# Kernel tuning notes

Measured on AMD Instinct MI355X. Metric: run time of the kernel, lower is better.

The kernel has to match this reference:

```python
import jax, jax.numpy as jnp
import numpy as np

VOCAB = 32000
D = 256        # embedding dim
NB = 256       # n_bubbles
NEQ = 5        # n_equilibrium_steps
THRESH = 1.5   # surprise_threshold
SEQ = 64
DECAYS = np.array([0.3, 0.7, 0.9], dtype=np.float32)  # RunningKnow frame decay rates


def setup_inputs() -> dict:
    key = jax.random.key(0)
    k1, k2, k3 = jax.random.split(key, 3)
    tokens = jax.random.randint(k1, (SEQ,), 0, VOCAB)
    E = jax.random.normal(k2, (VOCAB, D), dtype=jnp.float32)
    # Foam bubble measurement operators (stand-in: per-bubble linear map), scaled for sane stats
    W = jax.random.normal(k3, (NB, D, D), dtype=jnp.float32) / np.float32(np.sqrt(D))
    return {
        "tokens": tokens,
        "E": E,
        "W": W,
        "memory_decay_base": jnp.asarray(0.8, dtype=jnp.float32),
        "novelty_sensitivity": jnp.asarray(1.0, dtype=jnp.float32),
    }


def _equilibrate(m):
    # Stand-in for Foam.equilibrate: NEQ relaxation steps toward the bubble mean.
    for _ in range(NEQ):
        m = m + 0.1 * (m.mean(axis=0, keepdims=True) - m)
    return m


def reference(tokens, E, W, memory_decay_base, novelty_sensitivity):
    dr = jnp.asarray(DECAYS)[:, None, None]          # [F,1,1]
    F = dr.shape[0]
    sens = jnp.abs(novelty_sensitivity)

    def step(carry, tok):
        memory, means, vars_, n_seen = carry
        x = E[tok]                                   # [D]
        mm = memory.mean(axis=0)                     # [D]
        mem_norm = jnp.linalg.norm(mm) + 1e-10
        x_norm = jnp.linalg.norm(x) + 1e-10
        novelty = jnp.where(mem_norm > 1e-8,
                            1.0 - jnp.dot(x, mm) / (x_norm * mem_norm),
                            jnp.float32(1.0))
        decay = jax.nn.sigmoid(memory_decay_base - sens * novelty)
        xm = x + decay * mm                          # [D]

        meas = jnp.einsum('d,nde->ne', xm, W)        # [NB,D] bubble measurements

        # RunningKnow.evaluate (blank model at n_seen==0 -> never knows)
        std = jnp.sqrt(vars_ + 1e-8)                 # [F,NB,D]
        surprise = (jnp.abs(meas[None] - means) / std).mean(axis=(1, 2))  # [F]
        any_knows = jnp.any((surprise < THRESH) & (n_seen > 0))

        eq = _equilibrate(meas)
        eff = jnp.where(any_knows, meas, eq)         # know -> skip equilibration
        eff_d = jax.lax.stop_gradient(eff)           # .detach() in torch

        # RunningKnow.update (EMA mean/var per frame; first call initializes)
        upd_mean = dr * means + (1.0 - dr) * eff_d
        upd_var = jnp.maximum(dr * vars_ + (1.0 - dr) * (eff_d - means) * (eff_d - upd_mean), 1e-8)
        first = (n_seen == 0)
        means = jnp.where(first, jnp.broadcast_to(eff_d, (F, NB, D)), upd_mean)
        vars_ = jnp.where(first, jnp.float32(0.1), upd_var)

        # density matrix and spectrum
        mnorm = eff / (jnp.linalg.norm(eff, axis=-1, keepdims=True) + 1e-10)  # [NB,D]
        rho = mnorm.T @ mnorm / NB                   # [D,D]
        eigs = jnp.linalg.eigvalsh(jax.lax.stop_gradient(rho))
        eigs = jnp.maximum(eigs, 1e-12)
        eigs = eigs / eigs.sum()

        memory = decay * memory + (1.0 - decay) * eff_d
        logits = ((E @ rho) * E).sum(axis=-1)        # [VOCAB]
        return (memory, means, vars_, n_seen + 1), (logits, eigs)

    carry0 = (jnp.zeros((NB, D), jnp.float32),
              jnp.zeros((F, NB, D), jnp.float32),
              jnp.ones((F, NB, D), jnp.float32),
              jnp.int32(0))
    _, (logits, eigs) = jax.lax.scan(step, carry0, tokens)
    return logits, eigs  # [SEQ,VOCAB], [SEQ,D]
```

## Files before the change

### kernel.cpp

```cpp
#include <hip/hip_runtime.h>
#include <hip/hip_bf16.h>
#include <cstdint>
#include <cstddef>

constexpr size_t OFF_MEM    = 0;
constexpr size_t OFF_XM     = 65536;
constexpr size_t OFF_MU     = 82176;
constexpr size_t OFF_SABS   = 98560;
constexpr size_t OFF_BAR    = 98816;
constexpr size_t ZERO_END   = 98880;
constexpr size_t OFF_WBAR   = 98880;
constexpr size_t OFF_MEANS  = 164416;
constexpr size_t OFF_VARS   = 361024;
constexpr size_t OFF_DT     = 557632;
constexpr size_t OFF_ET     = 574016;
constexpr size_t OFF_RHO    = 590400;
constexpr size_t OFF_MN16   = 4784704;
constexpr size_t OFF_E16    = 6881856;
constexpr size_t WS_FLOATS  = 10977856;

#define SEQ_ 64
#define VOCAB_ 32000

typedef __attribute__((ext_vector_type(8))) short bf16x8;
typedef __attribute__((ext_vector_type(4))) float f32x4;

__device__ __forceinline__ float wave_sum(float v){
  v += __shfl_xor(v, 32); v += __shfl_xor(v, 16); v += __shfl_xor(v, 8);
  v += __shfl_xor(v, 4);  v += __shfl_xor(v, 2);  v += __shfl_xor(v, 1);
  return v;
}
__device__ __forceinline__ float block_sum(float v, float* red){
  int tid = threadIdx.x;
  v = wave_sum(v);
  if ((tid & 63) == 0) red[tid >> 6] = v;
  __syncthreads();
  float r = red[0] + red[1] + red[2] + red[3];
  __syncthreads();
  return r;
}
__device__ __forceinline__ float block_min(float v, float* red){
  int tid = threadIdx.x;
  v = fminf(v, __shfl_xor(v, 32)); v = fminf(v, __shfl_xor(v, 16));
  v = fminf(v, __shfl_xor(v, 8));  v = fminf(v, __shfl_xor(v, 4));
  v = fminf(v, __shfl_xor(v, 2));  v = fminf(v, __shfl_xor(v, 1));
  if ((tid & 63) == 0) red[tid >> 6] = v;
  __syncthreads();
  float r = fminf(fminf(red[0], red[1]), fminf(red[2], red[3]));
  __syncthreads();
  return r;
}
__device__ __forceinline__ float block_max(float v, float* red){
  int tid = threadIdx.x;
  v = fmaxf(v, __shfl_xor(v, 32)); v = fmaxf(v, __shfl_xor(v, 16));
  v = fmaxf(v, __shfl_xor(v, 8));  v = fmaxf(v, __shfl_xor(v, 4));
  v = fmaxf(v, __shfl_xor(v, 2));  v = fmaxf(v, __shfl_xor(v, 1));
  if ((tid & 63) == 0) red[tid >> 6] = v;
  __syncthreads();
  float r = fmaxf(fmaxf(red[0], red[1]), fmaxf(red[2], red[3]));
  __syncthreads();
  return r;
}

__global__ __launch_bounds__(256) void k0_init(const float* __restrict__ E, float* __restrict__ ws){
  size_t i = (size_t)blockIdx.x * 256 + threadIdx.x;
  if (i < ZERO_END) ws[i] = 0.f;
  __hip_bfloat16* e16 = (__hip_bfloat16*)(ws + OFF_E16);
  e16[i] = __float2bfloat16(E[i]);
}

__global__ __launch_bounds__(256) void k_wbar(const float* __restrict__ W, float* __restrict__ ws){
  size_t i = (size_t)blockIdx.x * 256 + threadIdx.x;
  float s = 0.f;
  #pragma unroll 4
  for (int n = 0; n < 256; ++n)
    s += W[(size_t)n * 65536 + i];
  ws[OFF_WBAR + i] = s * (1.0f / 256.0f);
}

__global__ __launch_bounds__(1024, 1) void k_xm(const int* __restrict__ tokens,
    const float* __restrict__ E, const float* __restrict__ mdbp,
    const float* __restrict__ nsp, float* __restrict__ ws){
  __shared__ float xm_s[256];
  __shared__ __align__(16) float part[4][256];
  __shared__ float redA[16], redB[16], redC[16];
  const int tid = threadIdx.x;
  const int e = tid & 255, q = tid >> 8;
  const int lane = tid & 63, w = tid >> 6;
  const float sens = fabsf(nsp[0]);
  const float mdb  = mdbp[0];
  const float* Wb = ws + OFF_WBAR;
  float mm = 0.f;

  float wreg[64];
  {
    const float* Wq = Wb + (size_t)(q * 64) * 256 + e;
    #pragma unroll
    for (int dd = 0; dd < 64; ++dd)
      wreg[dd] = Wq[(size_t)dd * 256];
  }

  for (int t = 0; t < SEQ_; ++t){
    int tok = tokens[t];
    float xv = (tid < 256) ? E[(size_t)tok * 256 + e] : 0.f;
    float a = wave_sum(xv * mm);
    float b = wave_sum(xv * xv);
    float c = wave_sum(mm * mm);
    if (lane == 0){ redA[w] = a; redB[w] = b; redC[w] = c; }
    __syncthreads();
    float sdot = (redA[0] + redA[1]) + (redA[2] + redA[3]);
    float sx2  = (redB[0] + redB[1]) + (redB[2] + redB[3]);
    float sm2  = (redC[0] + redC[1]) + (redC[2] + redC[3]);
    float mem_norm = sqrtf(sm2) + 1e-10f;
    float x_norm   = sqrtf(sx2) + 1e-10f;
    float novelty = (mem_norm > 1e-8f) ? (1.0f - sdot / (x_norm * mem_norm)) : 1.0f;
    float z = mdb - sens * novelty;
    float decay = 1.0f / (1.0f + expf(-z));
    if (tid < 256){
      float xmv = xv + decay * mm;
      xm_s[e] = xmv;
      ws[OFF_XM + (size_t)e * 64 + t] = xmv;
    }
    __syncthreads();

    float p = 0.f;
    #pragma unroll
    for (int dd = 0; dd < 64; ++dd)
      p = fmaf(xm_s[q * 64 + dd], wreg[dd], p);
    part[q][e] = p;
    __syncthreads();
    if (tid < 256){
      float acc = (part[0][e] + part[1][e]) + (part[2][e] + part[3][e]);
      ws[OFF_MU + (size_t)t * 256 + e] = acc;
      mm = decay * mm + (1.0f - decay) * acc;
    }
    __syncthreads();
  }
}

__global__ __launch_bounds__(256) void k_measall(const float* __restrict__ W, float* __restrict__ ws){
  __shared__ __align__(16) float xm_s[16384];
  const int tid = threadIdx.x, n = blockIdx.x;
  for (int i = tid; i < 16384; i += 256) xm_s[i] = ws[OFF_XM + i];
  __syncthreads();

  float acc[64];
  #pragma unroll
  for (int t = 0; t < 64; ++t) acc[t] = 0.f;

  const float* Wn = W + (size_t)n * 65536 + tid;
  for (int d = 0; d < 256; ++d){
    float wv = Wn[(size_t)d * 256];
    const float* xr = &xm_s[d * 64];
    #pragma unroll
    for (int q = 0; q < 16; ++q){
      float4 x4 = *(const float4*)&xr[q * 4];
      acc[q * 4 + 0] = fmaf(x4.x, wv, acc[q * 4 + 0]);
      acc[q * 4 + 1] = fmaf(x4.y, wv, acc[q * 4 + 1]);
      acc[q * 4 + 2] = fmaf(x4.z, wv, acc[q * 4 + 2]);
      acc[q * 4 + 3] = fmaf(x4.w, wv, acc[q * 4 + 3]);
    }
  }
  #pragma unroll
  for (int t = 0; t < 64; ++t)
    ws[OFF_RHO + (size_t)n * 16384 + (size_t)t * 256 + tid] = acc[t];
}

__global__ __launch_bounds__(1024, 1) void k_stats(float* __restrict__ ws){
  __shared__ float redA[16], redB[16], redC[16];
  const int tid = threadIdx.x;
  const int e = tid & 255, q = tid >> 8;
  const int lane = tid & 63, w = tid >> 6;
  const int n = blockIdx.x * 4 + q;
  unsigned* bar = (unsigned*)(ws + OFF_BAR);
  __hip_bfloat16* mn16 = (__hip_bfloat16*)(ws + OFF_MN16);
  const size_t ne = (size_t)n * 256 + e;
  const float TH = 1.5f * 65536.0f;
  const float c5 = 0.59049f;

  float mean0 = 0.f, mean1 = 0.f, mean2 = 0.f;
  float var0 = 0.f, var1 = 0.f, var2 = 0.f;

  for (int t = 0; t < SEQ_; ++t){
    float me = ws[OFF_RHO + (size_t)n * 16384 + (size_t)t * 256 + e];
    bool know = false;
    if (t > 0){
      float v0 = fabsf(me - mean0) / sqrtf(var0 + 1e-8f);
      float v1 = fabsf(me - mean1) / sqrtf(var1 + 1e-8f);
      float v2 = fabsf(me - mean2) / sqrtf(var2 + 1e-8f);
      float a = wave_sum(v0), b = wave_sum(v1), c = wave_sum(v2);
      if (lane == 0){ redA[w] = a; redB[w] = b; redC[w] = c; }
      __syncthreads();
      if (tid == 0){
        float sA = 0.f, sB = 0.f, sC = 0.f;
        #pragma unroll
        for (int i = 0; i < 16; ++i){ sA += redA[i]; sB += redB[i]; sC += redC[i]; }
        atomicAdd(&ws[OFF_SABS + (size_t)t * 4 + 0], sA);
        atomicAdd(&ws[OFF_SABS + (size_t)t * 4 + 1], sB);
        atomicAdd(&ws[OFF_SABS + (size_t)t * 4 + 2], sC);
        __hip_atomic_fetch_add(bar, 1u, __ATOMIC_ACQ_REL, __HIP_MEMORY_SCOPE_AGENT);
        unsigned tgt = 64u * (unsigned)t;
        while (__hip_atomic_load(bar, __ATOMIC_ACQUIRE, __HIP_MEMORY_SCOPE_AGENT) < tgt)
          __builtin_amdgcn_s_sleep(2);
      }
      __syncthreads();
      float s0 = __hip_atomic_load(&ws[OFF_SABS + (size_t)t * 4 + 0], __ATOMIC_RELAXED, __HIP_MEMORY_SCOPE_AGENT);
      float s1 = __hip_atomic_load(&ws[OFF_SABS + (size_t)t * 4 + 1], __ATOMIC_RELAXED, __HIP_MEMORY_SCOPE_AGENT);
      float s2 = __hip_atomic_load(&ws[OFF_SABS + (size_t)t * 4 + 2], __ATOMIC_RELAXED, __HIP_MEMORY_SCOPE_AGENT);
      know = (s0 < TH) || (s1 < TH) || (s2 < TH);
    }
    float mu = ws[OFF_MU + (size_t)t * 256 + e];
    float eq = c5 * me + (1.0f - c5) * mu;
    float eff = know ? me : eq;

    if (t == 0){
      mean0 = eff; mean1 = eff; mean2 = eff;
      var0 = 0.1f; var1 = 0.1f; var2 = 0.1f;
    } else {
      float um, uv;
      um = 0.3f * mean0 + 0.7f * eff;
      uv = 0.3f * var0 + 0.7f * (eff - mean0) * (eff - um);
      mean0 = um; var0 = fmaxf(uv, 1e-8f);
      um = 0.7f * mean1 + 0.3f * eff;
      uv = 0.7f * var1 + 0.3f * (eff - mean1) * (eff - um);
      mean1 = um; var1 = fmaxf(uv, 1e-8f);
      um = 0.9f * mean2 + 0.1f * eff;
      uv = 0.9f * var2 + 0.1f * (eff - mean2) * (eff - um);
      mean2 = um; var2 = fmaxf(uv, 1e-8f);
    }

    float nv = wave_sum(eff * eff);
    if (lane == 0) redA[w] = nv;
    __syncthreads();
    float nr2 = (redA[4 * q + 0] + redA[4 * q + 1]) + (redA[4 * q + 2] + redA[4 * q + 3]);
    float rn = sqrtf(nr2) + 1e-10f;
    mn16[(size_t)t * 65536 + ne] = __float2bfloat16(eff / rn);
    __syncthreads();
  }
}

__global__ __launch_bounds__(256) void k_rho(float* __restrict__ ws){
  const int t = blockIdx.x, rb = blockIdx.y, tid = threadIdx.x;
  __shared__ __align__(16) float tile[32][256];
  const unsigned short* mn16 = (const unsigned short*)(ws + OFF_MN16);
  float acc[32];
  #pragma unroll
  for (int i = 0; i < 32; ++i) acc[i] = 0.f;
  for (int c = 0; c < 8; ++c){
    __syncthreads();
    #pragma unroll
    for (int v = 0; v < 4; ++v){
      int idx = v * 256 + tid;
      int row = idx >> 5, c16 = idx & 31;
      uint4 u4 = *(const uint4*)(mn16 + (size_t)t * 65536 + (size_t)(c * 32 + row) * 256 + c16 * 8);
      float* dst = &tile[row][c16 * 8];
      unsigned uu[4] = {u4.x, u4.y, u4.z, u4.w};
      #pragma unroll
      for (int j = 0; j < 4; ++j){
        dst[j * 2 + 0] = __uint_as_float(uu[j] << 16);
        dst[j * 2 + 1] = __uint_as_float(uu[j] & 0xffff0000u);
      }
    }
    __syncthreads();
    for (int nl = 0; nl < 32; ++nl){
      float ev = tile[nl][tid];
      #pragma unroll
      for (int q = 0; q < 8; ++q){
        float4 dv = *(const float4*)&tile[nl][rb * 32 + q * 4];
        acc[q * 4 + 0] = fmaf(dv.x, ev, acc[q * 4 + 0]);
        acc[q * 4 + 1] = fmaf(dv.y, ev, acc[q * 4 + 1]);
        acc[q * 4 + 2] = fmaf(dv.z, ev, acc[q * 4 + 2]);
        acc[q * 4 + 3] = fmaf(dv.w, ev, acc[q * 4 + 3]);
      }
    }
  }
  #pragma unroll
  for (int i = 0; i < 32; ++i)
    ws[OFF_RHO + (size_t)t * 65536 + (size_t)(rb * 32 + i) * 256 + tid] = acc[i] * (1.0f / 256.0f);
}

__global__ __launch_bounds__(512, 2) void k_trigemm(float* __restrict__ ws, float* __restrict__ out){
  __shared__ __align__(16) char smem_raw[51200];
  const int tid = threadIdx.x;

  if (blockIdx.x < 64){
    float* ca   = (float*)smem_raw;
    float* ua   = ca + 256;
    float* wa   = ua + 256;
    float* ph   = wa + 256;
    float* redA = ph + 512;
    float* redB = redA + 8;
    const int t = blockIdx.x;
    const int c = tid & 255, h = tid >> 8;
    const float* rho = ws + OFF_RHO + (size_t)t * 65536;
    float* dT = ws + OFF_DT + (size_t)t * 256;
    float* eT = ws + OFF_ET + (size_t)t * 256;

    float Mreg[128];
    {
      const float* Mc = rho + (size_t)(h * 128) * 256 + c;
      #pragma unroll
      for (int rr = 0; rr < 128; ++rr)
        Mreg[rr] = Mc[(size_t)rr * 256];
    }
    const int rowbase = h * 128;

    for (int k = 0; k < 254; ++k){
      __syncthreads();
      if (c == k){
        #pragma unroll
        for (int rr = 0; rr < 128; ++rr) ca[rowbase + rr] = Mreg[rr];
      }
      __syncthreads();
      float uval = 0.f;
      if (tid < 256){
        float raw = ca[tid];
        uval = (tid > k) ? raw : 0.f;
        ua[tid] = uval;
        if (tid == 0) dT[k] = ca[k];
      }
      float pa = wave_sum(uval * uval);
      if ((tid & 63) == 0) redA[tid >> 6] = pa;
      __syncthreads();
      float sigma2 = redA[0] + redA[1] + redA[2] + redA[3]
                   + redA[4] + redA[5] + redA[6] + redA[7];
      float v0 = ca[k + 1];
      if (sigma2 < 1e-30f){
        if (tid == 0) eT[k] = v0;
        continue;
      }
      float sig = sqrtf(sigma2);
      float alpha = (v0 >= 0.f) ? -sig : sig;
      float u0 = v0 - alpha;
      float beta = 2.0f / (sigma2 - v0 * v0 + u0 * u0);
      if (tid == 0) eT[k] = alpha;
      if (tid == k + 1) ua[tid] = u0;
      __syncthreads();

      {
        float a0 = 0.f, a1 = 0.f, a2 = 0.f, a3 = 0.f;
        #pragma unroll
        for (int rr = 0; rr < 128; rr += 4){
          float4 u4 = *(const float4*)&ua[rowbase + rr];
          a0 = fmaf(Mreg[rr + 0], u4.x, a0);
          a1 = fmaf(Mreg[rr + 1], u4.y, a1);
          a2 = fmaf(Mreg[rr + 2], u4.z, a2);
          a3 = fmaf(Mreg[rr + 3], u4.w, a3);
        }
        ph[tid] = (a0 + a1) + (a2 + a3);
      }
      __syncthreads();
      float p = ph[c] + ph[c + 256];
      float up = (tid < 256) ? ua[tid] * p : 0.f;
      float pb = wave_sum(up);
      if ((tid & 63) == 0) redB[tid >> 6] = pb;
      __syncthreads();
      float s = redB[0] + redB[1] + redB[2] + redB[3]
              + redB[4] + redB[5] + redB[6] + redB[7];
      if (tid < 256) wa[tid] = (tid > k) ? (beta * p - 0.5f * beta * beta * s * ua[tid]) : 0.f;
      __syncthreads();
      {
        float ucv = ua[c], wcv = wa[c];
        #pragma unroll
        for (int rr = 0; rr < 128; rr += 4){
          float4 u4 = *(const float4*)&ua[rowbase + rr];
          float4 w4 = *(const float4*)&wa[rowbase + rr];
          Mreg[rr + 0] = fmaf(-w4.x, ucv, fmaf(-u4.x, wcv, Mreg[rr + 0]));
          Mreg[rr + 1] = fmaf(-w4.y, ucv, fmaf(-u4.y, wcv, Mreg[rr + 1]));
          Mreg[rr + 2] = fmaf(-w4.z, ucv, fmaf(-u4.z, wcv, Mreg[rr + 2]));
          Mreg[rr + 3] = fmaf(-w4.w, ucv, fmaf(-u4.w, wcv, Mreg[rr + 3]));
        }
      }
    }

    __syncthreads();
    if (c == 254){
      #pragma unroll
      for (int rr = 0; rr < 128; ++rr) ca[rowbase + rr] = Mreg[rr];
    }
    __syncthreads();
    if (tid == 0){ dT[254] = ca[254]; eT[254] = ca[255]; }
    __syncthreads();
    if (c == 255){
      #pragma unroll
      for (int rr = 0; rr < 128; ++rr) ca[rowbase + rr] = Mreg[rr];
    }
    __syncthreads();
    if (tid == 0){ dT[255] = ca[255]; eT[255] = 0.f; }
  } else {
    short* A_lds = (short*)smem_raw;
    short* B_lds = A_lds + 8192;
    float* pl    = (float*)(B_lds + 16384);
    const int g = blockIdx.x - 64;
    const int bx = g % 250, t = g / 250;
    const int lane = tid & 63, w = tid >> 6;
    const int wr = w >> 2, wc = w & 3;
    const int vbase = bx * 128;
    const short* E16 = (const short*)(ws + OFF_E16);
    const short* MN  = (const short*)(ws + OFF_MN16) + (size_t)t * 65536;

    f32x4 acc[4][4];
    #pragma unroll
    for (int i = 0; i < 4; ++i)
      #pragma unroll
      for (int j = 0; j < 4; ++j){ f32x4 z = {0.f, 0.f, 0.f, 0.f}; acc[i][j] = z; }

    const int gq = lane >> 4, r16 = lane & 15;
    const int sx = r16 & 7;
    for (int it = 0; it < 4; ++it){
      const int k0 = it * 64;
      __syncthreads();
      #pragma unroll
      for (int pa = 0; pa < 2; ++pa){
        int ch = pa * 512 + tid;
        int row = ch >> 3, c8 = ch & 7;
        int sc8 = c8 ^ (row & 7);
        uint4 v = *(const uint4*)(E16 + (size_t)(vbase + row) * 256 + k0 + sc8 * 8);
        *(uint4*)&A_lds[ch * 8] = v;
      }
      #pragma unroll
      for (int pb = 0; pb < 4; ++pb){
        int ch = pb * 512 + tid;
        int row = ch >> 3, c8 = ch & 7;
        int sc8 = c8 ^ (row & 7);
        uint4 v = *(const uint4*)(MN + (size_t)row * 256 + k0 + sc8 * 8);
        *(uint4*)&B_lds[ch * 8] = v;
      }
      __syncthreads();
      #pragma unroll
      for (int kk = 0; kk < 64; kk += 32){
        const int j0 = (kk >> 3) + gq;
        bf16x8 af[4], bf[4];
        #pragma unroll
        for (int fm = 0; fm < 4; ++fm)
          af[fm] = *(const bf16x8*)&A_lds[(wr * 64 + fm * 16 + r16) * 64 + (j0 ^ sx) * 8];
        #pragma unroll
        for (int fn = 0; fn < 4; ++fn)
          bf[fn] = *(const bf16x8*)&B_lds[(wc * 64 + fn * 16 + r16) * 64 + (j0 ^ sx) * 8];
        #pragma unroll
        for (int fm = 0; fm < 4; ++fm)
          #pragma unroll
          for (int fn = 0; fn < 4; ++fn)
            acc[fm][fn] = __builtin_amdgcn_mfma_f32_16x16x32_bf16(af[fm], bf[fn], acc[fm][fn], 0, 0, 0);
      }
    }

    float ps[4][4];
    #pragma unroll
    for (int fm = 0; fm < 4; ++fm)
      #pragma unroll
      for (int i = 0; i < 4; ++i){
        float sv = 0.f;
        #pragma unroll
        for (int fn = 0; fn < 4; ++fn){ float v = acc[fm][fn][i]; sv += v * v; }
        sv += __shfl_xor(sv, 1); sv += __shfl_xor(sv, 2);
        sv += __shfl_xor(sv, 4); sv += __shfl_xor(sv, 8);
        ps[fm][i] = sv;
      }
    __syncthreads();
    if (r16 == 0){
      #pragma unroll
      for (int fm = 0; fm < 4; ++fm)
        #pragma unroll
        for (int i = 0; i < 4; ++i)
          pl[w * 64 + fm * 16 + gq * 4 + i] = ps[fm][i];
    }
    __syncthreads();
    if (tid < 128){
      int rr = tid;
      int wrr = rr >> 6, lr = rr & 63;
      float sum = pl[(wrr * 4 + 0) * 64 + lr] + pl[(wrr * 4 + 1) * 64 + lr]
                + pl[(wrr * 4 + 2) * 64 + lr] + pl[(wrr * 4 + 3) * 64 + lr];
      out[(size_t)t * VOCAB_ + vbase + rr] = sum * (1.0f / 256.0f);
    }
  }
}

__global__ __launch_bounds__(256) void k_bisect(const float* __restrict__ ws, float* __restrict__ out){
  __shared__ float d_s[256];
  __shared__ float e2_s[256];
  __shared__ float ea_s[256];
  __shared__ float red[4];
  const int t = blockIdx.x, tid = threadIdx.x;
  d_s[tid] = ws[OFF_DT + (size_t)t * 256 + tid];
  float evv = (tid < 255) ? ws[OFF_ET + (size_t)t * 256 + tid] : 0.f;
  e2_s[tid] = evv * evv;
  ea_s[tid] = fabsf(evv);
  __syncthreads();
  float rad = ea_s[tid] + ((tid > 0) ? ea_s[tid - 1] : 0.f);
  float glo = block_min(d_s[tid] - rad, red);
  float ghi = block_max(d_s[tid] + rad, red);

  float l = glo, h = ghi;
  for (int it = 0; it < 40; ++it){
    float mid = 0.5f * (l + h);
    float q = d_s[0] - mid;
    int cnt = (q < 0.f) ? 1 : 0;
    #pragma unroll 8
    for (int i = 1; i < 256; ++i){
      float qr = __builtin_amdgcn_rcpf(q);
      q = (d_s[i] - mid) - e2_s[i - 1] * qr;
      q = (fabsf(q) < 1e-25f) ? -1e-25f : q;
      cnt += (q < 0.f) ? 1 : 0;
    }
    if (cnt <= tid) l = mid; else h = mid;
  }
  float lam = fmaxf(0.5f * (l + h), 1e-12f);
  float ssum = block_sum(lam, red);
  out[(size_t)SEQ_ * VOCAB_ + (size_t)t * 256 + tid] = lam / ssum;
}

extern "C" void kernel_launch(void* const* d_in, const int* in_sizes, int n_in,
                              void* d_out, int out_size, void* d_ws, size_t ws_size,
                              hipStream_t stream){
  const int*   tokens = (const int*)d_in[0];
  const float* E      = (const float*)d_in[1];
  const float* W      = (const float*)d_in[2];
  const float* mdbp   = (const float*)d_in[3];
  const float* nsp    = (const float*)d_in[4];
  float* out = (float*)d_out;
  float* ws  = (float*)d_ws;
  if (ws_size < WS_FLOATS * sizeof(float)) return;

  k0_init<<<dim3(32000), dim3(256), 0, stream>>>(E, ws);
  k_wbar<<<dim3(256), dim3(256), 0, stream>>>(W, ws);
  k_xm<<<dim3(1), dim3(1024), 0, stream>>>(tokens, E, mdbp, nsp, ws);
  k_measall<<<dim3(256), dim3(256), 0, stream>>>(W, ws);
  {
    void* args[1];
    args[0] = (void*)&ws;
    hipLaunchCooperativeKernel((const void*)k_stats, dim3(64), dim3(1024), args, 0, stream);
  }
  k_rho<<<dim3(64, 8), dim3(256), 0, stream>>>(ws);
  k_trigemm<<<dim3(64 + 250 * 64), dim3(512), 0, stream>>>(ws, out);
  k_bisect<<<dim3(64), dim3(256), 0, stream>>>(ws, out);
}
```

Before: 3.070 ms.

## Replace atomic surprise sums with per-block partials, fuse wbar into init kernel

In the cooperative stats kernel, each block now stores its three per-frame surprise partial sums into its own slot instead of doing float atomicAdds on one shared location. After the grid barrier every wave reads all 64 slots and reduces them with a wave reduction. A separate reduction buffer is used so a trailing __syncthreads per step can be dropped, and one barrier is removed in k_xm. The W-mean reduction is folded into the init kernel to save a launch, at the cost of idle branches in most init blocks and dependence on a subtle reasoning about barrier removal safety.

```diff
diff --git a/kernel.cpp b/kernel.cpp
--- a/kernel.cpp
+++ b/kernel.cpp
@@ -62,20 +62,19 @@
   return r;
 }
 
-__global__ __launch_bounds__(256) void k0_init(const float* __restrict__ E, float* __restrict__ ws){
+__global__ __launch_bounds__(256) void k0_init(const float* __restrict__ E,
+    const float* __restrict__ W, float* __restrict__ ws){
   size_t i = (size_t)blockIdx.x * 256 + threadIdx.x;
   if (i < ZERO_END) ws[i] = 0.f;
   __hip_bfloat16* e16 = (__hip_bfloat16*)(ws + OFF_E16);
   e16[i] = __float2bfloat16(E[i]);
-}
-
-__global__ __launch_bounds__(256) void k_wbar(const float* __restrict__ W, float* __restrict__ ws){
-  size_t i = (size_t)blockIdx.x * 256 + threadIdx.x;
-  float s = 0.f;
-  #pragma unroll 4
-  for (int n = 0; n < 256; ++n)
-    s += W[(size_t)n * 65536 + i];
-  ws[OFF_WBAR + i] = s * (1.0f / 256.0f);
+  if (blockIdx.x < 256){
+    float s = 0.f;
+    #pragma unroll 4
+    for (int n = 0; n < 256; ++n)
+      s += W[(size_t)n * 65536 + i];
+    ws[OFF_WBAR + i] = s * (1.0f / 256.0f);
+  }
 }
 
 __global__ __launch_bounds__(1024, 1) void k_xm(const int* __restrict__ tokens,
@@ -134,7 +133,6 @@
       ws[OFF_MU + (size_t)t * 256 + e] = acc;
       mm = decay * mm + (1.0f - decay) * acc;
     }
-    __syncthreads();
   }
 }
 
@@ -167,12 +165,13 @@
 }
 
 __global__ __launch_bounds__(1024, 1) void k_stats(float* __restrict__ ws){
-  __shared__ float redA[16], redB[16], redC[16];
+  __shared__ float redA[16], redB[16], redC[16], redD[16];
   const int tid = threadIdx.x;
   const int e = tid & 255, q = tid >> 8;
   const int lane = tid & 63, w = tid >> 6;
   const int n = blockIdx.x * 4 + q;
   unsigned* bar = (unsigned*)(ws + OFF_BAR);
+  float* sabsP = ws + OFF_MEANS;
   __hip_bfloat16* mn16 = (__hip_bfloat16*)(ws + OFF_MN16);
   const size_t ne = (size_t)n * 256 + e;
   const float TH = 1.5f * 65536.0f;
@@ -195,18 +194,23 @@
         float sA = 0.f, sB = 0.f, sC = 0.f;
         #pragma unroll
         for (int i = 0; i < 16; ++i){ sA += redA[i]; sB += redB[i]; sC += redC[i]; }
-        atomicAdd(&ws[OFF_SABS + (size_t)t * 4 + 0], sA);
-        atomicAdd(&ws[OFF_SABS + (size_t)t * 4 + 1], sB);
-        atomicAdd(&ws[OFF_SABS + (size_t)t * 4 + 2], sC);
+        size_t base = (size_t)t * 192 + blockIdx.x;
+        __hip_atomic_store(&sabsP[base],       sA, __ATOMIC_RELAXED, __HIP_MEMORY_SCOPE_AGENT);
+        __hip_atomic_store(&sabsP[base + 64],  sB, __ATOMIC_RELAXED, __HIP_MEMORY_SCOPE_AGENT);
+        __hip_atomic_store(&sabsP[base + 128], sC, __ATOMIC_RELAXED, __HIP_MEMORY_SCOPE_AGENT);
         __hip_atomic_fetch_add(bar, 1u, __ATOMIC_ACQ_REL, __HIP_MEMORY_SCOPE_AGENT);
         unsigned tgt = 64u * (unsigned)t;
         while (__hip_atomic_load(bar, __ATOMIC_ACQUIRE, __HIP_MEMORY_SCOPE_AGENT) < tgt)
           __builtin_amdgcn_s_sleep(2);
       }
       __syncthreads();
-      float s0 = __hip_atomic_load(&ws[OFF_SABS + (size_t)t * 4 + 0], __ATOMIC_RELAXED, __HIP_MEMORY_SCOPE_AGENT);
-      float s1 = __hip_atomic_load(&ws[OFF_SABS + (size_t)t * 4 + 1], __ATOMIC_RELAXED, __HIP_MEMORY_SCOPE_AGENT);
-      float s2 = __hip_atomic_load(&ws[OFF_SABS + (size_t)t * 4 + 2], __ATOMIC_RELAXED, __HIP_MEMORY_SCOPE_AGENT);
+      size_t pbase = (size_t)t * 192;
+      float p0 = __hip_atomic_load(&sabsP[pbase + lane],       __ATOMIC_RELAXED, __HIP_MEMORY_SCOPE_AGENT);
+      float p1 = __hip_atomic_load(&sabsP[pbase + 64 + lane],  __ATOMIC_RELAXED, __HIP_MEMORY_SCOPE_AGENT);
+      float p2 = __hip_atomic_load(&sabsP[pbase + 128 + lane], __ATOMIC_RELAXED, __HIP_MEMORY_SCOPE_AGENT);
+      float s0 = wave_sum(p0);
+      float s1 = wave_sum(p1);
+      float s2 = wave_sum(p2);
       know = (s0 < TH) || (s1 < TH) || (s2 < TH);
     }
     float mu = ws[OFF_MU + (size_t)t * 256 + e];
@@ -230,12 +234,11 @@
     }
 
     float nv = wave_sum(eff * eff);
-    if (lane == 0) redA[w] = nv;
-    __syncthreads();
-    float nr2 = (redA[4 * q + 0] + redA[4 * q + 1]) + (redA[4 * q + 2] + redA[4 * q + 3]);
+    if (lane == 0) redD[w] = nv;
+    __syncthreads();
+    float nr2 = (redD[4 * q + 0] + redD[4 * q + 1]) + (redD[4 * q + 2] + redD[4 * q + 3]);
     float rn = sqrtf(nr2) + 1e-10f;
     mn16[(size_t)t * 65536 + ne] = __float2bfloat16(eff / rn);
-    __syncthreads();
   }
 }
 
@@ -522,8 +525,7 @@
   float* ws  = (float*)d_ws;
   if (ws_size < WS_FLOATS * sizeof(float)) return;
 
-  k0_init<<<dim3(32000), dim3(256), 0, stream>>>(E, ws);
-  k_wbar<<<dim3(256), dim3(256), 0, stream>>>(W, ws);
+  k0_init<<<dim3(32000), dim3(256), 0, stream>>>(E, W, ws);
   k_xm<<<dim3(1), dim3(1024), 0, stream>>>(tokens, E, mdbp, nsp, ws);
   k_measall<<<dim3(256), dim3(256), 0, stream>>>(W, ws);
   {
```

After: 2.940 ms. -4.2%, faster.
